# Optimization experiments

Hardware: AMD Instinct MI355X
Metric: run time of the kernel (lower is better)

Reference implementation:

```python
import jax, jax.numpy as jnp
import numpy as np


def setup_inputs() -> dict:
    key = jax.random.key(0)
    ks = jax.random.split(key, 7)
    B, D, N, R = 256, 5120, 16, 160  # batch, d_inner, d_state, dt_rank
    x = jax.random.normal(ks[0], (B, D), jnp.float32)
    h0 = jax.random.normal(ks[1], (B, D, N), jnp.float32)
    W_x_dt = jax.random.normal(ks[2], (D, R), jnp.float32) * (1.0 / np.sqrt(D))
    W_dt = jax.random.normal(ks[3], (R, D), jnp.float32) * (1.0 / np.sqrt(R))
    b_dt = jax.random.normal(ks[4], (D,), jnp.float32)
    W_BC = jax.random.normal(ks[5], (D, 2 * N), jnp.float32) * (1.0 / np.sqrt(D))
    A_log = jax.random.normal(ks[6], (D, N), jnp.float32)
    return {"x": x, "h0": h0, "W_x_dt": W_x_dt, "W_dt": W_dt,
            "b_dt": b_dt, "W_BC": W_BC, "A_log": A_log}


def reference(x, h0, W_x_dt, W_dt, b_dt, W_BC, A_log):
    # Single-token Mamba selective SSM step (batch dims squeezed: x [B,D], h0 [B,D,N]).
    N = A_log.shape[1]
    # delta_t = softplus(dt_proj(delta_t_proj(x)))  -> [B, D]
    dt = jax.nn.softplus((x @ W_x_dt) @ W_dt + b_dt)
    # BC projection, split into B and C parts -> [B, N] each
    BC = x @ W_BC
    Bm, Cm = BC[:, :N], BC[:, N:]
    A = -jnp.exp(A_log)                              # [D, N]
    delta_A = jnp.exp(A[None, :, :] * dt[:, :, None])   # [B, D, N]
    delta_Bx = (dt * x)[:, :, None] * Bm[:, None, :]     # [B, D, N]
    h = delta_A * h0 + delta_Bx                          # new hidden state
    # y = h @ C (per-batch bmm over state dim) + x residual
    y = jnp.einsum('bdn,bn->bd', h, Cm) + x              # [B, D]
    return y
```

## Files before the change

### kernel.cpp

```cpp
#include <hip/hip_runtime.h>
#include <math.h>

#define BB 256
#define DD 5120
#define NN 16
#define RR 160
#define CT 192
#define NSPLIT 64
#define KSPL 80
#define TMP_ELEMS (BB * CT)

__global__ __launch_bounds__(256) void k1_gemm(const float* __restrict__ x,
                                               const float* __restrict__ Wxdt,
                                               const float* __restrict__ Wbc,
                                               float* __restrict__ part) {
    __shared__ float xs[16][68];
    __shared__ float ws[16][64];
    const int tid = threadIdx.x;
    const int tx = tid & 15, ty = tid >> 4;
    const int c0 = blockIdx.x * 64;
    const int b0 = blockIdx.y * 64;
    const int k0 = blockIdx.z * KSPL;
    float acc[4][4] = {};

    for (int kc = 0; kc < KSPL; kc += 16) {
        {
            const int row = tid >> 2;
            const int j4  = (tid & 3) * 4;
            const float4 v = *(const float4*)&x[(size_t)(b0 + row) * DD + k0 + kc + j4];
            xs[j4 + 0][row] = v.x;
            xs[j4 + 1][row] = v.y;
            xs[j4 + 2][row] = v.z;
            xs[j4 + 3][row] = v.w;
        }
        {
            const int r  = tid >> 4;
            const int c4 = (tid & 15) * 4;
            const int kg = k0 + kc + r;
            const int cg = c0 + c4;
            float4 v;
            if (cg < RR) v = *(const float4*)&Wxdt[(size_t)kg * RR + cg];
            else         v = *(const float4*)&Wbc[(size_t)kg * 32 + (cg - RR)];
            *(float4*)&ws[r][c4] = v;
        }
        __syncthreads();
        #pragma unroll
        for (int k = 0; k < 16; ++k) {
            const float4 a4 = *(const float4*)&xs[k][ty * 4];
            const float4 w4 = *(const float4*)&ws[k][tx * 4];
            const float av[4] = {a4.x, a4.y, a4.z, a4.w};
            const float wv[4] = {w4.x, w4.y, w4.z, w4.w};
            #pragma unroll
            for (int u = 0; u < 4; ++u)
                #pragma unroll
                for (int v = 0; v < 4; ++v)
                    acc[u][v] = fmaf(av[u], wv[v], acc[u][v]);
        }
        __syncthreads();
    }

    float* p = part + (size_t)blockIdx.z * TMP_ELEMS;
    #pragma unroll
    for (int u = 0; u < 4; ++u) {
        const int b = b0 + ty * 4 + u;
        *(float4*)&p[b * CT + c0 + tx * 4] =
            make_float4(acc[u][0], acc[u][1], acc[u][2], acc[u][3]);
    }
}

__global__ __launch_bounds__(256) void k_red(const float* __restrict__ part,
                                             float* __restrict__ tmp) {
    const int idx = blockIdx.x * 256 + threadIdx.x;
    float s = 0.f;
    #pragma unroll
    for (int z = 0; z < NSPLIT; ++z) s += part[(size_t)z * TMP_ELEMS + idx];
    tmp[idx] = s;
}

__global__ __launch_bounds__(256) void k2_dt(const float* __restrict__ tmp,
                                             const float* __restrict__ Wdt,
                                             const float* __restrict__ bdt,
                                             float* __restrict__ dt) {
    __shared__ float ts[32][34];
    __shared__ float ws[32][64];
    const int tid = threadIdx.x;
    const int tx = tid & 15, ty = tid >> 4;
    const int d0 = blockIdx.x * 64;
    const int b0 = blockIdx.y * 32;
    float acc[2][4] = {};

    for (int kc = 0; kc < RR; kc += 32) {
        {
            const int row = tid >> 3;
            const int j4  = (tid & 7) * 4;
            const float4 v = *(const float4*)&tmp[(size_t)(b0 + row) * CT + kc + j4];
            ts[j4 + 0][row] = v.x;
            ts[j4 + 1][row] = v.y;
            ts[j4 + 2][row] = v.z;
            ts[j4 + 3][row] = v.w;
        }
        {
            const int c4 = (tid & 15) * 4;
            const int r0 = tid >> 4;
            #pragma unroll
            for (int rep = 0; rep < 2; ++rep) {
                const int r = r0 + rep * 16;
                *(float4*)&ws[r][c4] = *(const float4*)&Wdt[(size_t)(kc + r) * DD + d0 + c4];
            }
        }
        __syncthreads();
        #pragma unroll
        for (int k = 0; k < 32; ++k) {
            const float a0 = ts[k][ty * 2 + 0];
            const float a1 = ts[k][ty * 2 + 1];
            const float4 w4 = *(const float4*)&ws[k][tx * 4];
            const float wv[4] = {w4.x, w4.y, w4.z, w4.w};
            #pragma unroll
            for (int v = 0; v < 4; ++v) {
                acc[0][v] = fmaf(a0, wv[v], acc[0][v]);
                acc[1][v] = fmaf(a1, wv[v], acc[1][v]);
            }
        }
        __syncthreads();
    }

    const float4 bv = *(const float4*)&bdt[d0 + tx * 4];
    const float bb[4] = {bv.x, bv.y, bv.z, bv.w};
    #pragma unroll
    for (int u = 0; u < 2; ++u) {
        const int b = b0 + ty * 2 + u;
        float o[4];
        #pragma unroll
        for (int v = 0; v < 4; ++v) {
            const float z = acc[u][v] + bb[v];
            o[v] = fmaxf(z, 0.f) + log1pf(__expf(-fabsf(z)));
        }
        *(float4*)&dt[(size_t)b * DD + d0 + tx * 4] = make_float4(o[0], o[1], o[2], o[3]);
    }
}

__global__ __launch_bounds__(256) void k3_ssm(const float* __restrict__ x,
                                              const float* __restrict__ h0,
                                              const float* __restrict__ dt,
                                              const float* __restrict__ tmp,
                                              const float* __restrict__ Alog,
                                              float* __restrict__ out) {
    const int tid = threadIdx.x;
    const int q = tid >> 2;
    const int l = tid & 3;
    const int d = blockIdx.x * 64 + q;
    const int b0 = blockIdx.y * 16;

    const float4 av = *(const float4*)&Alog[(size_t)d * NN + l * 4];
    const float na[4] = {-__expf(av.x), -__expf(av.y), -__expf(av.z), -__expf(av.w)};

    #pragma unroll 4
    for (int bi = 0; bi < 16; ++bi) {
        const int b = b0 + bi;
        const size_t bd = (size_t)b * DD + d;
        const float4 h4 = *(const float4*)&h0[bd * NN + l * 4];
        const float dtv = dt[bd];
        const float xv  = x[bd];
        const float4 bm4 = *(const float4*)&tmp[(size_t)b * CT + RR + l * 4];
        const float4 cm4 = *(const float4*)&tmp[(size_t)b * CT + RR + 16 + l * 4];
        const float dtx = dtv * xv;

        float p0, p1;
        p0 = fmaf(__expf(na[0] * dtv), h4.x, dtx * bm4.x) * cm4.x;
        p1 = fmaf(__expf(na[1] * dtv), h4.y, dtx * bm4.y) * cm4.y;
        p0 = fmaf(fmaf(__expf(na[2] * dtv), h4.z, dtx * bm4.z), cm4.z, p0);
        p1 = fmaf(fmaf(__expf(na[3] * dtv), h4.w, dtx * bm4.w), cm4.w, p1);
        float p = p0 + p1;
        p += __shfl_xor(p, 1);
        p += __shfl_xor(p, 2);
        if (l == 0) out[bd] = xv + p;
    }
}

extern "C" void kernel_launch(void* const* d_in, const int* in_sizes, int n_in,
                              void* d_out, int out_size, void* d_ws, size_t ws_size,
                              hipStream_t stream) {
    const float* x    = (const float*)d_in[0];
    const float* h0   = (const float*)d_in[1];
    const float* Wxdt = (const float*)d_in[2];
    const float* Wdt  = (const float*)d_in[3];
    const float* bdt  = (const float*)d_in[4];
    const float* Wbc  = (const float*)d_in[5];
    const float* Alog = (const float*)d_in[6];
    float* out = (float*)d_out;

    float* part  = (float*)d_ws;
    float* tmp   = part + (size_t)NSPLIT * TMP_ELEMS;
    float* dtbuf = tmp + TMP_ELEMS;

    k1_gemm<<<dim3(3, 4, NSPLIT), 256, 0, stream>>>(x, Wxdt, Wbc, part);
    k_red<<<dim3(TMP_ELEMS / 256), 256, 0, stream>>>(part, tmp);
    k2_dt<<<dim3(DD / 64, BB / 32), 256, 0, stream>>>(tmp, Wdt, bdt, dtbuf);
    k3_ssm<<<dim3(DD / 64, BB / 16), 256, 0, stream>>>(x, h0, dtbuf, tmp, Alog, out);
}
```

Baseline: 188.2 us.

## Fuse four kernels into persistent megakernel with atomic grid barriers

Merges the split-K GEMM, partial reduction, dt projection and SSM step kernels into one persistent kernel of 768 blocks, separated by software grid barriers built on atomic counters. A small init kernel resets the counters. The goal is to remove the launch gaps and tail effects between four dependent kernels. The cost is spin-wait barrier overhead, and the barriers deadlock if all 768 blocks cannot be resident at once. The SSM phase also has fewer blocks, each looping over tiles.

```diff
diff --git a/kernel.cpp b/kernel.cpp
--- a/kernel.cpp
+++ b/kernel.cpp
@@ -9,171 +9,198 @@
 #define NSPLIT 64
 #define KSPL 80
 #define TMP_ELEMS (BB * CT)
-
-__global__ __launch_bounds__(256) void k1_gemm(const float* __restrict__ x,
+#define NBLK 768
+#define CTR_STRIDE 32
+
+__global__ void kinit(int* ctr) {
+    if (threadIdx.x < 3) ctr[threadIdx.x * CTR_STRIDE] = 0;
+}
+
+__device__ __forceinline__ void gbar(int* ctr) {
+    __syncthreads();
+    if (threadIdx.x == 0) {
+        __threadfence();
+        __hip_atomic_fetch_add(ctr, 1, __ATOMIC_RELEASE, __HIP_MEMORY_SCOPE_AGENT);
+        while (__hip_atomic_load(ctr, __ATOMIC_ACQUIRE, __HIP_MEMORY_SCOPE_AGENT) < NBLK) {
+            __builtin_amdgcn_s_sleep(2);
+        }
+        __threadfence();
+    }
+    __syncthreads();
+}
+
+__global__ __launch_bounds__(256, 3) void mega(const float* __restrict__ x,
+                                               const float* __restrict__ h0,
                                                const float* __restrict__ Wxdt,
+                                               const float* __restrict__ Wdt,
+                                               const float* __restrict__ bdt,
                                                const float* __restrict__ Wbc,
-                                               float* __restrict__ part) {
-    __shared__ float xs[16][68];
-    __shared__ float ws[16][64];
+                                               const float* __restrict__ Alog,
+                                               float* __restrict__ out,
+                                               float* __restrict__ part,
+                                               float* __restrict__ tmp,
+                                               float* __restrict__ dtb,
+                                               int* __restrict__ ctr) {
+    __shared__ float smem[32 * 34 + 32 * 64];
     const int tid = threadIdx.x;
-    const int tx = tid & 15, ty = tid >> 4;
-    const int c0 = blockIdx.x * 64;
-    const int b0 = blockIdx.y * 64;
-    const int k0 = blockIdx.z * KSPL;
-    float acc[4][4] = {};
-
-    for (int kc = 0; kc < KSPL; kc += 16) {
-        {
-            const int row = tid >> 2;
-            const int j4  = (tid & 3) * 4;
-            const float4 v = *(const float4*)&x[(size_t)(b0 + row) * DD + k0 + kc + j4];
-            xs[j4 + 0][row] = v.x;
-            xs[j4 + 1][row] = v.y;
-            xs[j4 + 2][row] = v.z;
-            xs[j4 + 3][row] = v.w;
-        }
-        {
-            const int r  = tid >> 4;
-            const int c4 = (tid & 15) * 4;
-            const int kg = k0 + kc + r;
-            const int cg = c0 + c4;
-            float4 v;
-            if (cg < RR) v = *(const float4*)&Wxdt[(size_t)kg * RR + cg];
-            else         v = *(const float4*)&Wbc[(size_t)kg * 32 + (cg - RR)];
-            *(float4*)&ws[r][c4] = v;
-        }
-        __syncthreads();
+    const int bid = blockIdx.x;
+
+    {
+        float* xs = smem;
+        float* ws = smem + 16 * 68;
+        const int tx = tid & 15, ty = tid >> 4;
+        const int c0 = (bid % 3) * 64;
+        const int b0 = ((bid / 3) & 3) * 64;
+        const int s  = bid / 12;
+        const int k0 = s * KSPL;
+        float acc[4][4] = {};
+
+        for (int kc = 0; kc < KSPL; kc += 16) {
+            {
+                const int row = tid >> 2;
+                const int j4  = (tid & 3) * 4;
+                const float4 v = *(const float4*)&x[(size_t)(b0 + row) * DD + k0 + kc + j4];
+                xs[(j4 + 0) * 68 + row] = v.x;
+                xs[(j4 + 1) * 68 + row] = v.y;
+                xs[(j4 + 2) * 68 + row] = v.z;
+                xs[(j4 + 3) * 68 + row] = v.w;
+            }
+            {
+                const int r  = tid >> 4;
+                const int c4 = (tid & 15) * 4;
+                const int kg = k0 + kc + r;
+                const int cg = c0 + c4;
+                float4 v;
+                if (cg < RR) v = *(const float4*)&Wxdt[(size_t)kg * RR + cg];
+                else         v = *(const float4*)&Wbc[(size_t)kg * 32 + (cg - RR)];
+                *(float4*)&ws[r * 64 + c4] = v;
+            }
+            __syncthreads();
+            #pragma unroll
+            for (int k = 0; k < 16; ++k) {
+                const float4 a4 = *(const float4*)&xs[k * 68 + ty * 4];
+                const float4 w4 = *(const float4*)&ws[k * 64 + tx * 4];
+                const float av[4] = {a4.x, a4.y, a4.z, a4.w};
+                const float wv[4] = {w4.x, w4.y, w4.z, w4.w};
+                #pragma unroll
+                for (int u = 0; u < 4; ++u)
+                    #pragma unroll
+                    for (int v = 0; v < 4; ++v)
+                        acc[u][v] = fmaf(av[u], wv[v], acc[u][v]);
+            }
+            __syncthreads();
+        }
+        float* p = part + (size_t)s * TMP_ELEMS;
         #pragma unroll
-        for (int k = 0; k < 16; ++k) {
-            const float4 a4 = *(const float4*)&xs[k][ty * 4];
-            const float4 w4 = *(const float4*)&ws[k][tx * 4];
-            const float av[4] = {a4.x, a4.y, a4.z, a4.w};
-            const float wv[4] = {w4.x, w4.y, w4.z, w4.w};
-            #pragma unroll
-            for (int u = 0; u < 4; ++u)
+        for (int u = 0; u < 4; ++u) {
+            const int b = b0 + ty * 4 + u;
+            *(float4*)&p[b * CT + c0 + tx * 4] =
+                make_float4(acc[u][0], acc[u][1], acc[u][2], acc[u][3]);
+        }
+    }
+    gbar(&ctr[0 * CTR_STRIDE]);
+
+    {
+        const int idx = bid * 256 + tid;
+        if (idx < TMP_ELEMS) {
+            float sum = 0.f;
+            #pragma unroll
+            for (int z = 0; z < NSPLIT; ++z) sum += part[(size_t)z * TMP_ELEMS + idx];
+            tmp[idx] = sum;
+        }
+    }
+    gbar(&ctr[1 * CTR_STRIDE]);
+
+    if (bid < 640) {
+        float* ts  = smem;
+        float* wsd = smem + 32 * 34;
+        const int tx = tid & 15, ty = tid >> 4;
+        const int d0 = (bid % 80) * 64;
+        const int b0 = (bid / 80) * 32;
+        float acc[2][4] = {};
+
+        for (int kc = 0; kc < RR; kc += 32) {
+            {
+                const int row = tid >> 3;
+                const int j4  = (tid & 7) * 4;
+                const float4 v = *(const float4*)&tmp[(size_t)(b0 + row) * CT + kc + j4];
+                ts[(j4 + 0) * 34 + row] = v.x;
+                ts[(j4 + 1) * 34 + row] = v.y;
+                ts[(j4 + 2) * 34 + row] = v.z;
+                ts[(j4 + 3) * 34 + row] = v.w;
+            }
+            {
+                const int c4 = (tid & 15) * 4;
+                const int r0 = tid >> 4;
                 #pragma unroll
-                for (int v = 0; v < 4; ++v)
-                    acc[u][v] = fmaf(av[u], wv[v], acc[u][v]);
-        }
-        __syncthreads();
-    }
-
-    float* p = part + (size_t)blockIdx.z * TMP_ELEMS;
-    #pragma unroll
-    for (int u = 0; u < 4; ++u) {
-        const int b = b0 + ty * 4 + u;
-        *(float4*)&p[b * CT + c0 + tx * 4] =
-            make_float4(acc[u][0], acc[u][1], acc[u][2], acc[u][3]);
-    }
-}
-
-__global__ __launch_bounds__(256) void k_red(const float* __restrict__ part,
-                                             float* __restrict__ tmp) {
-    const int idx = blockIdx.x * 256 + threadIdx.x;
-    float s = 0.f;
-    #pragma unroll
-    for (int z = 0; z < NSPLIT; ++z) s += part[(size_t)z * TMP_ELEMS + idx];
-    tmp[idx] = s;
-}
-
-__global__ __launch_bounds__(256) void k2_dt(const float* __restrict__ tmp,
-                                             const float* __restrict__ Wdt,
-                                             const float* __restrict__ bdt,
-                                             float* __restrict__ dt) {
-    __shared__ float ts[32][34];
-    __shared__ float ws[32][64];
-    const int tid = threadIdx.x;
-    const int tx = tid & 15, ty = tid >> 4;
-    const int d0 = blockIdx.x * 64;
-    const int b0 = blockIdx.y * 32;
-    float acc[2][4] = {};
-
-    for (int kc = 0; kc < RR; kc += 32) {
-        {
-            const int row = tid >> 3;
-            const int j4  = (tid & 7) * 4;
-            const float4 v = *(const float4*)&tmp[(size_t)(b0 + row) * CT + kc + j4];
-            ts[j4 + 0][row] = v.x;
-            ts[j4 + 1][row] = v.y;
-            ts[j4 + 2][row] = v.z;
-            ts[j4 + 3][row] = v.w;
-        }
-        {
-            const int c4 = (tid & 15) * 4;
-            const int r0 = tid >> 4;
-            #pragma unroll
-            for (int rep = 0; rep < 2; ++rep) {
-                const int r = r0 + rep * 16;
-                *(float4*)&ws[r][c4] = *(const float4*)&Wdt[(size_t)(kc + r) * DD + d0 + c4];
-            }
-        }
-        __syncthreads();
+                for (int rep = 0; rep < 2; ++rep) {
+                    const int r = r0 + rep * 16;
+                    *(float4*)&wsd[r * 64 + c4] =
+                        *(const float4*)&Wdt[(size_t)(kc + r) * DD + d0 + c4];
+                }
+            }
+            __syncthreads();
+            #pragma unroll
+            for (int k = 0; k < 32; ++k) {
+                const float a0 = ts[k * 34 + ty * 2 + 0];
+                const float a1 = ts[k * 34 + ty * 2 + 1];
+                const float4 w4 = *(const float4*)&wsd[k * 64 + tx * 4];
+                const float wv[4] = {w4.x, w4.y, w4.z, w4.w};
+                #pragma unroll
+                for (int v = 0; v < 4; ++v) {
+                    acc[0][v] = fmaf(a0, wv[v], acc[0][v]);
+                    acc[1][v] = fmaf(a1, wv[v], acc[1][v]);
+                }
+            }
+            __syncthreads();
+        }
+        const float4 bv = *(const float4*)&bdt[d0 + tx * 4];
+        const float bb[4] = {bv.x, bv.y, bv.z, bv.w};
         #pragma unroll
-        for (int k = 0; k < 32; ++k) {
-            const float a0 = ts[k][ty * 2 + 0];
-            const float a1 = ts[k][ty * 2 + 1];
-            const float4 w4 = *(const float4*)&ws[k][tx * 4];
-            const float wv[4] = {w4.x, w4.y, w4.z, w4.w};
+        for (int u = 0; u < 2; ++u) {
+            const int b = b0 + ty * 2 + u;
+            float o[4];
             #pragma unroll
             for (int v = 0; v < 4; ++v) {
-                acc[0][v] = fmaf(a0, wv[v], acc[0][v]);
-                acc[1][v] = fmaf(a1, wv[v], acc[1][v]);
-            }
-        }
-        __syncthreads();
-    }
-
-    const float4 bv = *(const float4*)&bdt[d0 + tx * 4];
-    const float bb[4] = {bv.x, bv.y, bv.z, bv.w};
-    #pragma unroll
-    for (int u = 0; u < 2; ++u) {
-        const int b = b0 + ty * 2 + u;
-        float o[4];
-        #pragma unroll
-        for (int v = 0; v < 4; ++v) {
-            const float z = acc[u][v] + bb[v];
-            o[v] = fmaxf(z, 0.f) + log1pf(__expf(-fabsf(z)));
-        }
-        *(float4*)&dt[(size_t)b * DD + d0 + tx * 4] = make_float4(o[0], o[1], o[2], o[3]);
-    }
-}
-
-__global__ __launch_bounds__(256) void k3_ssm(const float* __restrict__ x,
-                                              const float* __restrict__ h0,
-                                              const float* __restrict__ dt,
-                                              const float* __restrict__ tmp,
-                                              const float* __restrict__ Alog,
-                                              float* __restrict__ out) {
-    const int tid = threadIdx.x;
-    const int q = tid >> 2;
-    const int l = tid & 3;
-    const int d = blockIdx.x * 64 + q;
-    const int b0 = blockIdx.y * 16;
-
-    const float4 av = *(const float4*)&Alog[(size_t)d * NN + l * 4];
-    const float na[4] = {-__expf(av.x), -__expf(av.y), -__expf(av.z), -__expf(av.w)};
-
-    #pragma unroll 4
-    for (int bi = 0; bi < 16; ++bi) {
-        const int b = b0 + bi;
-        const size_t bd = (size_t)b * DD + d;
-        const float4 h4 = *(const float4*)&h0[bd * NN + l * 4];
-        const float dtv = dt[bd];
-        const float xv  = x[bd];
-        const float4 bm4 = *(const float4*)&tmp[(size_t)b * CT + RR + l * 4];
-        const float4 cm4 = *(const float4*)&tmp[(size_t)b * CT + RR + 16 + l * 4];
-        const float dtx = dtv * xv;
-
-        float p0, p1;
-        p0 = fmaf(__expf(na[0] * dtv), h4.x, dtx * bm4.x) * cm4.x;
-        p1 = fmaf(__expf(na[1] * dtv), h4.y, dtx * bm4.y) * cm4.y;
-        p0 = fmaf(fmaf(__expf(na[2] * dtv), h4.z, dtx * bm4.z), cm4.z, p0);
-        p1 = fmaf(fmaf(__expf(na[3] * dtv), h4.w, dtx * bm4.w), cm4.w, p1);
-        float p = p0 + p1;
-        p += __shfl_xor(p, 1);
-        p += __shfl_xor(p, 2);
-        if (l == 0) out[bd] = xv + p;
+                const float z = acc[u][v] + bb[v];
+                o[v] = fmaxf(z, 0.f) + log1pf(__expf(-fabsf(z)));
+            }
+            *(float4*)&dtb[(size_t)b * DD + d0 + tx * 4] = make_float4(o[0], o[1], o[2], o[3]);
+        }
+    }
+    gbar(&ctr[2 * CTR_STRIDE]);
+
+    {
+        const int q = tid >> 2;
+        const int l = tid & 3;
+        for (int t = bid; t < 1280; t += NBLK) {
+            const int d  = (t % 80) * 64 + q;
+            const int b0 = (t / 80) * 16;
+            const float4 av = *(const float4*)&Alog[(size_t)d * NN + l * 4];
+            const float na[4] = {-__expf(av.x), -__expf(av.y), -__expf(av.z), -__expf(av.w)};
+
+            #pragma unroll 4
+            for (int bi = 0; bi < 16; ++bi) {
+                const int b = b0 + bi;
+                const size_t bd = (size_t)b * DD + d;
+                const float4 h4 = *(const float4*)&h0[bd * NN + l * 4];
+                const float dtv = dtb[bd];
+                const float xv  = x[bd];
+                const float4 bm4 = *(const float4*)&tmp[(size_t)b * CT + RR + l * 4];
+                const float4 cm4 = *(const float4*)&tmp[(size_t)b * CT + RR + 16 + l * 4];
+                const float dtx = dtv * xv;
+
+                float p0, p1;
+                p0 = fmaf(__expf(na[0] * dtv), h4.x, dtx * bm4.x) * cm4.x;
+                p1 = fmaf(__expf(na[1] * dtv), h4.y, dtx * bm4.y) * cm4.y;
+                p0 = fmaf(fmaf(__expf(na[2] * dtv), h4.z, dtx * bm4.z), cm4.z, p0);
+                p1 = fmaf(fmaf(__expf(na[3] * dtv), h4.w, dtx * bm4.w), cm4.w, p1);
+                float p = p0 + p1;
+                p += __shfl_xor(p, 1);
+                p += __shfl_xor(p, 2);
+                if (l == 0) out[bd] = xv + p;
+            }
+        }
     }
 }
 
@@ -189,12 +216,12 @@
     const float* Alog = (const float*)d_in[6];
     float* out = (float*)d_out;
 
-    float* part  = (float*)d_ws;
-    float* tmp   = part + (size_t)NSPLIT * TMP_ELEMS;
-    float* dtbuf = tmp + TMP_ELEMS;
-
-    k1_gemm<<<dim3(3, 4, NSPLIT), 256, 0, stream>>>(x, Wxdt, Wbc, part);
-    k_red<<<dim3(TMP_ELEMS / 256), 256, 0, stream>>>(part, tmp);
-    k2_dt<<<dim3(DD / 64, BB / 32), 256, 0, stream>>>(tmp, Wdt, bdt, dtbuf);
-    k3_ssm<<<dim3(DD / 64, BB / 16), 256, 0, stream>>>(x, h0, dtbuf, tmp, Alog, out);
-}
+    float* part = (float*)d_ws;
+    float* tmp  = part + (size_t)NSPLIT * TMP_ELEMS;
+    float* dtb  = tmp + TMP_ELEMS;
+    int*   ctr  = (int*)(dtb + (size_t)BB * DD);
+
+    kinit<<<1, 64, 0, stream>>>(ctr);
+    mega<<<dim3(NBLK), dim3(256), 0, stream>>>(x, h0, Wxdt, Wdt, bdt, Wbc, Alog,
+                                               out, part, tmp, dtb, ctr);
+}
```

Result: slower. 521.9 us (+177.3%).
